# Kernel optimization log

Hardware: AMD Instinct MI355X
Metric: run time of the kernel (lower is better)

The kernel has to match this reference:

```python
import jax, jax.numpy as jnp
import numpy as np

N, M = 50000, 2048          # nodes, observations
E, O = 512, 256             # in_features_embed, in_features_obs
EPS = 1e-6


def setup_inputs() -> dict:
    key = jax.random.key(0)
    k1, k2, k3, k4, k5 = jax.random.split(key, 5)
    scale_e = 1.0 / np.sqrt(E)
    scale_o = 1.0 / np.sqrt(O)
    return {
        "node_feature": jax.random.normal(k1, (N, E), dtype=jnp.float32),
        "obs_feature": jax.random.normal(k2, (M, O), dtype=jnp.float32),
        # nn.Linear weights, stored as [out, in] like torch
        "W_q": jax.random.normal(k3, (E, E), dtype=jnp.float32) * scale_e,
        "W_k": jax.random.normal(k4, (E, O), dtype=jnp.float32) * scale_o,
        "W_v": jax.random.normal(k5, (E, O), dtype=jnp.float32) * scale_o,
        "ln_gamma": jnp.ones((E,), dtype=jnp.float32),
        "ln_beta": jnp.zeros((E,), dtype=jnp.float32),
    }


def layer_norm(x, gamma, beta, eps=EPS):
    mu = jnp.mean(x, axis=-1, keepdims=True)
    var = jnp.mean(jnp.square(x - mu), axis=-1, keepdims=True)
    return (x - mu) * jax.lax.rsqrt(var + eps) * gamma + beta


def reference(node_feature, obs_feature, W_q, W_k, W_v, ln_gamma, ln_beta):
    # projections (torch Linear: x @ W.T)
    q = node_feature @ W_q.T            # [N, E]
    k = obs_feature @ W_k.T             # [M, E]
    v = obs_feature @ W_v.T             # [M, E]
    # un-normalized cross-attention (no softmax), original association
    attn = q @ k.T                      # [N, M]
    out = attn @ v                      # [N, E]
    return layer_norm(out + node_feature, ln_gamma, ln_beta)
```

## Files before the change

kernel.cpp:

```cpp
#include <hip/hip_runtime.h>
#include <hip/hip_bf16.h>

#define NROWS 50000
#define MOBS  2048
#define EDIM  512
#define ODIM  256
#define BM2   128
#define NT2   391

typedef short s16x8 __attribute__((ext_vector_type(8)));
typedef float f32x4 __attribute__((ext_vector_type(4)));

typedef const __attribute__((address_space(1))) unsigned int* gptr_t;
typedef __attribute__((address_space(3))) unsigned int* lptr_t;

__device__ __forceinline__ unsigned short f32_to_bf16(float f) {
    unsigned int u = __float_as_uint(f);
    u += 0x7fffu + ((u >> 16) & 1u);
    return (unsigned short)(u >> 16);
}

__device__ __forceinline__ s16x8 pack8(f32x4 a, f32x4 b) {
    unsigned int p0, p1, p2, p3;
    asm("v_cvt_pk_bf16_f32 %0, %1, %2" : "=v"(p0) : "v"(a[0]), "v"(a[1]));
    asm("v_cvt_pk_bf16_f32 %0, %1, %2" : "=v"(p1) : "v"(a[2]), "v"(a[3]));
    asm("v_cvt_pk_bf16_f32 %0, %1, %2" : "=v"(p2) : "v"(b[0]), "v"(b[1]));
    asm("v_cvt_pk_bf16_f32 %0, %1, %2" : "=v"(p3) : "v"(b[2]), "v"(b[3]));
    union { unsigned int u[4]; s16x8 v; } r;
    r.u[0] = p0; r.u[1] = p1; r.u[2] = p2; r.u[3] = p3;
    return r.v;
}

__global__ __launch_bounds__(256) void chain1(const float* __restrict__ obs,
                                              const float* __restrict__ Wq,
                                              const float* __restrict__ Wk,
                                              float* __restrict__ Gp,
                                              float* __restrict__ Pp) {
    __shared__ float SA[16][68];
    __shared__ float SB[16][68];
    const int b = blockIdx.x;
    const float *A, *B;
    float* C;
    int lda, ldb, k_lo, k_hi, i0, j0;
    if (b < 128) {
        int z = b >> 4, tile = b & 15;
        i0 = (tile >> 2) * 64; j0 = (tile & 3) * 64;
        A = obs; B = obs; C = Gp + (size_t)z * 65536;
        lda = ODIM; ldb = ODIM;
        k_lo = z * 256; k_hi = k_lo + 256;
    } else {
        int i2 = b - 128;
        int z = i2 >> 5, tile = i2 & 31;
        i0 = (tile >> 2) * 64; j0 = (tile & 3) * 64;
        A = Wq; B = Wk; C = Pp + (size_t)z * 131072;
        lda = EDIM; ldb = ODIM;
        k_lo = z * 128; k_hi = k_lo + 128;
    }
    const int t  = threadIdx.x;
    const int tx = t & 15, ty = t >> 4;

    float acc[4][4];
#pragma unroll
    for (int a = 0; a < 4; ++a)
#pragma unroll
        for (int c2 = 0; c2 < 4; ++c2) acc[a][c2] = 0.f;

    for (int k0 = k_lo; k0 < k_hi; k0 += 16) {
#pragma unroll
        for (int r = 0; r < 4; ++r) {
            int idx = t + 256 * r;
            int mm = idx & 63, kk2 = idx >> 6;
            SA[kk2][mm] = A[(size_t)(k0 + kk2) * lda + i0 + mm];
        }
#pragma unroll
        for (int r = 0; r < 4; ++r) {
            int idx = t + 256 * r;
            int jj = idx & 63, kk2 = idx >> 6;
            SB[kk2][jj] = B[(size_t)(k0 + kk2) * ldb + j0 + jj];
        }
        __syncthreads();
#pragma unroll
        for (int kk2 = 0; kk2 < 16; ++kk2) {
            float4 a4 = *(const float4*)&SA[kk2][ty * 4];
            float4 b4 = *(const float4*)&SB[kk2][tx * 4];
            float av[4] = {a4.x, a4.y, a4.z, a4.w};
            float bv[4] = {b4.x, b4.y, b4.z, b4.w};
#pragma unroll
            for (int a = 0; a < 4; ++a)
#pragma unroll
                for (int c2 = 0; c2 < 4; ++c2) acc[a][c2] += av[a] * bv[c2];
        }
        __syncthreads();
    }
#pragma unroll
    for (int a = 0; a < 4; ++a) {
        float4 o = make_float4(acc[a][0], acc[a][1], acc[a][2], acc[a][3]);
        *(float4*)&C[(size_t)(i0 + ty * 4 + a) * ODIM + j0 + tx * 4] = o;
    }
}

__global__ __launch_bounds__(256) void chain2(const float* __restrict__ Gp,
                                              const float* __restrict__ Wv,
                                              float* __restrict__ GW) {
    __shared__ float SA[16][68];
    __shared__ float SB[16][68];
    const int t  = threadIdx.x;
    const int tx = t & 15, ty = t >> 4;
    const int i0 = blockIdx.y * 64, j0 = blockIdx.x * 64;

    float acc[4][4];
#pragma unroll
    for (int a = 0; a < 4; ++a)
#pragma unroll
        for (int c2 = 0; c2 < 4; ++c2) acc[a][c2] = 0.f;

    for (int k0 = 0; k0 < ODIM; k0 += 16) {
#pragma unroll
        for (int r = 0; r < 4; ++r) {
            int idx = t + 256 * r;
            int kk2 = idx & 15, mm = idx >> 4;
            size_t off = (size_t)(i0 + mm) * ODIM + k0 + kk2;
            float v = 0.f;
#pragma unroll
            for (int z = 0; z < 8; ++z) v += Gp[off + (size_t)z * 65536];
            SA[kk2][mm] = v;
        }
#pragma unroll
        for (int r = 0; r < 4; ++r) {
            int idx = t + 256 * r;
            int kk2 = idx & 15, jj = idx >> 4;
            SB[kk2][jj] = Wv[(size_t)(j0 + jj) * ODIM + k0 + kk2];
        }
        __syncthreads();
#pragma unroll
        for (int kk2 = 0; kk2 < 16; ++kk2) {
            float4 a4 = *(const float4*)&SA[kk2][ty * 4];
            float4 b4 = *(const float4*)&SB[kk2][tx * 4];
            float av[4] = {a4.x, a4.y, a4.z, a4.w};
            float bv[4] = {b4.x, b4.y, b4.z, b4.w};
#pragma unroll
            for (int a = 0; a < 4; ++a)
#pragma unroll
                for (int c2 = 0; c2 < 4; ++c2) acc[a][c2] += av[a] * bv[c2];
        }
        __syncthreads();
    }
#pragma unroll
    for (int a = 0; a < 4; ++a) {
        float4 o = make_float4(acc[a][0], acc[a][1], acc[a][2], acc[a][3]);
        *(float4*)&GW[(size_t)(i0 + ty * 4 + a) * EDIM + j0 + tx * 4] = o;
    }
}

__global__ __launch_bounds__(256) void chain3(const float* __restrict__ Pp,
                                              const float* __restrict__ GW,
                                              unsigned short* __restrict__ Uf) {
    __shared__ float SA[16][68];
    __shared__ float SB[16][68];
    const int t  = threadIdx.x;
    const int tx = t & 15, ty = t >> 4;
    const int i0 = blockIdx.y * 64, j0 = blockIdx.x * 64;

    float acc[4][4];
#pragma unroll
    for (int a = 0; a < 4; ++a)
#pragma unroll
        for (int c2 = 0; c2 < 4; ++c2) acc[a][c2] = 0.f;

    for (int k0 = 0; k0 < ODIM; k0 += 16) {
#pragma unroll
        for (int r = 0; r < 4; ++r) {
            int idx = t + 256 * r;
            int kk2 = idx & 15, mm = idx >> 4;
            size_t off = (size_t)(i0 + mm) * ODIM + k0 + kk2;
            float v = 0.f;
#pragma unroll
            for (int z = 0; z < 4; ++z) v += Pp[off + (size_t)z * 131072];
            SA[kk2][mm] = v;
        }
#pragma unroll
        for (int r = 0; r < 4; ++r) {
            int idx = t + 256 * r;
            int jj = idx & 63, kk2 = idx >> 6;
            SB[kk2][jj] = GW[(size_t)(k0 + kk2) * EDIM + j0 + jj];
        }
        __syncthreads();
#pragma unroll
        for (int kk2 = 0; kk2 < 16; ++kk2) {
            float4 a4 = *(const float4*)&SA[kk2][ty * 4];
            float4 b4 = *(const float4*)&SB[kk2][tx * 4];
            float av[4] = {a4.x, a4.y, a4.z, a4.w};
            float bv[4] = {b4.x, b4.y, b4.z, b4.w};
#pragma unroll
            for (int a = 0; a < 4; ++a)
#pragma unroll
                for (int c2 = 0; c2 < 4; ++c2) acc[a][c2] += av[a] * bv[c2];
        }
        __syncthreads();
    }
#pragma unroll
    for (int a = 0; a < 4; ++a)
#pragma unroll
        for (int c2 = 0; c2 < 4; ++c2) {
            int i = i0 + ty * 4 + a;
            int j = j0 + tx * 4 + c2;
            float v = acc[a][c2] + (i == j ? 1.f : 0.f);
            size_t idx = ((size_t)(((i >> 5) * 32 + (j >> 4)) * 64
                           + ((i >> 3) & 3) * 16 + (j & 15))) * 8 + (i & 7);
            Uf[idx] = f32_to_bf16(v);
        }
}

__global__ __launch_bounds__(512, 2) void gemm_pipe_ln(
    const float* __restrict__ node, const unsigned short* __restrict__ Uf,
    const float* __restrict__ gamma, const float* __restrict__ beta,
    float* __restrict__ out) {
    __shared__ char smem[147456];
    char* Areg = smem;
    char* Breg = smem + 49152;
    float* lds_s  = (float*)smem;
    float* lds_q  = (float*)smem + 512;
    float* lds_mu = (float*)smem + 1024;
    float* lds_rs = (float*)smem + 1152;

    const int t  = threadIdx.x;
    const int w  = t >> 6, l = t & 63;
    const int rg = w >> 2, cg = w & 3;
    const int lr = l & 15, lk = l >> 4;
    const int m0 = blockIdx.x * BM2;

    const int sr = w * 8 + (l >> 3);
    const int schunk = (l & 7) ^ ((l >> 3) & 7);
    int gr0 = m0 + sr;      if (gr0 > NROWS - 1) gr0 = NROWS - 1;
    int gr1 = m0 + sr + 64; if (gr1 > NROWS - 1) gr1 = NROWS - 1;
    const char* asrc0 = (const char*)node + (size_t)gr0 * 2048 + schunk * 16;
    const char* asrc1 = (const char*)node + (size_t)gr1 * 2048 + schunk * 16;
    const char* bsrc  = (const char*)Uf + (size_t)w * 4096 + (size_t)l * 16;

    auto dma = [&](int buf, int kt) {
        char* ad = Areg + buf * 16384 + w * 1024;
        __builtin_amdgcn_global_load_lds((gptr_t)(asrc0 + kt * 128),
                                         (lptr_t)ad, 16, 0, 0);
        __builtin_amdgcn_global_load_lds((gptr_t)(asrc1 + kt * 128),
                                         (lptr_t)(ad + 8192), 16, 0, 0);
        char* bd = Breg + buf * 32768 + w * 4096;
        const char* bs = bsrc + (size_t)kt * 32768;
#pragma unroll
        for (int j = 0; j < 4; ++j)
            __builtin_amdgcn_global_load_lds((gptr_t)(bs + j * 1024),
                                             (lptr_t)(bd + j * 1024), 16, 0, 0);
    };

    f32x4 acc[4][8];
#pragma unroll
    for (int mi = 0; mi < 4; ++mi)
#pragma unroll
        for (int ni = 0; ni < 8; ++ni)
            acc[mi][ni] = (f32x4){0.f, 0.f, 0.f, 0.f};

    auto compute = [&](int cur) {
        const char* bbase = Breg + cur * 32768 + cg * 8192 + l * 16;
        s16x8 bfr[8];
#pragma unroll
        for (int ni = 0; ni < 8; ++ni)
            bfr[ni] = *(const s16x8*)(bbase + ni * 1024);
        s16x8 afr[4];
#pragma unroll
        for (int mi = 0; mi < 4; ++mi) {
            int row = rg * 64 + mi * 16 + lr;
            const char* rb = Areg + cur * 16384 + row * 128;
            f32x4 a0 = *(const f32x4*)(rb + ((2 * lk)     ^ (lr & 7)) * 16);
            f32x4 a1 = *(const f32x4*)(rb + ((2 * lk + 1) ^ (lr & 7)) * 16);
            afr[mi] = pack8(a0, a1);
        }
#pragma unroll
        for (int mi = 0; mi < 4; ++mi)
#pragma unroll
            for (int ni = 0; ni < 8; ++ni)
                acc[mi][ni] = __builtin_amdgcn_mfma_f32_16x16x32_bf16(
                    afr[mi], bfr[ni], acc[mi][ni], 0, 0, 0);
    };

    dma(0, 0);
    dma(1, 1);

#pragma unroll 1
    for (int kt = 0; kt < 14; ++kt) {
        dma((kt + 2) % 3, kt + 2);
        asm volatile("s_waitcnt vmcnt(12)" ::: "memory");
        __builtin_amdgcn_sched_barrier(0);
        __builtin_amdgcn_s_barrier();
        compute(kt % 3);
        __builtin_amdgcn_s_barrier();
    }
    asm volatile("s_waitcnt vmcnt(6)" ::: "memory");
    __builtin_amdgcn_sched_barrier(0);
    __builtin_amdgcn_s_barrier();
    compute(14 % 3);
    __builtin_amdgcn_s_barrier();
    asm volatile("s_waitcnt vmcnt(0)" ::: "memory");
    __builtin_amdgcn_sched_barrier(0);
    __builtin_amdgcn_s_barrier();
    compute(15 % 3);
    __syncthreads();

#pragma unroll
    for (int mi = 0; mi < 4; ++mi) {
#pragma unroll
        for (int j = 0; j < 4; ++j) {
            float sm = 0.f, q = 0.f;
#pragma unroll
            for (int ni = 0; ni < 8; ++ni) {
                float v = acc[mi][ni][j];
                sm += v; q += v * v;
            }
#pragma unroll
            for (int off = 1; off < 16; off <<= 1) {
                sm += __shfl_xor(sm, off);
                q  += __shfl_xor(q, off);
            }
            if (lr == 0) {
                int row = rg * 64 + mi * 16 + lk * 4 + j;
                lds_s[cg * 128 + row] = sm;
                lds_q[cg * 128 + row] = q;
            }
        }
    }
    __syncthreads();
    if (t < 128) {
        float sm = lds_s[t] + lds_s[128 + t] + lds_s[256 + t] + lds_s[384 + t];
        float q  = lds_q[t] + lds_q[128 + t] + lds_q[256 + t] + lds_q[384 + t];
        float mu  = sm * (1.f / (float)EDIM);
        float var = q * (1.f / (float)EDIM) - mu * mu;
        lds_mu[t] = mu;
        lds_rs[t] = rsqrtf(var + 1e-6f);
    }
    __syncthreads();

    float gv[8], bv[8];
#pragma unroll
    for (int ni = 0; ni < 8; ++ni) {
        int col = cg * 128 + ni * 16 + lr;
        gv[ni] = gamma[col];
        bv[ni] = beta[col];
    }

#pragma unroll
    for (int mi = 0; mi < 4; ++mi) {
#pragma unroll
        for (int j = 0; j < 4; ++j) {
            int row = rg * 64 + mi * 16 + lk * 4 + j;
            int gr = m0 + row;
            if (gr < NROWS) {
                float mu = lds_mu[row], rs = lds_rs[row];
                float* op = out + (size_t)gr * EDIM + cg * 128 + lr;
#pragma unroll
                for (int ni = 0; ni < 8; ++ni)
                    op[ni * 16] = (acc[mi][ni][j] - mu) * rs * gv[ni] + bv[ni];
            }
        }
    }
}

extern "C" void kernel_launch(void* const* d_in, const int* in_sizes, int n_in,
                              void* d_out, int out_size, void* d_ws, size_t ws_size,
                              hipStream_t stream) {
    const float* node  = (const float*)d_in[0];
    const float* obs   = (const float*)d_in[1];
    const float* Wq    = (const float*)d_in[2];
    const float* Wk    = (const float*)d_in[3];
    const float* Wv    = (const float*)d_in[4];
    const float* gamma = (const float*)d_in[5];
    const float* beta  = (const float*)d_in[6];
    float* out = (float*)d_out;

    float* ws = (float*)d_ws;
    float* Gp = ws;
    float* Pp = Gp + 8 * 65536;
    float* GW = Pp + 4 * 131072;
    unsigned short* Uf = (unsigned short*)(GW + ODIM * EDIM);

    chain1<<<dim3(256), 256, 0, stream>>>(obs, Wq, Wk, Gp, Pp);
    chain2<<<dim3(8, 4), 256, 0, stream>>>(Gp, Wv, GW);
    chain3<<<dim3(8, 8), 256, 0, stream>>>(Pp, GW, Uf);
    gemm_pipe_ln<<<dim3(NT2), 512, 0, stream>>>(node, Uf, gamma, beta, out);
}
```

Baseline: 120.0 us.

## Unify small chain GEMMs with register-prefetched float4 loads and K=32 tiles

The three small fp32 GEMM kernels that build the fused weight matrix are replaced by one templated 64x64 tile routine. It loads tiles with float4 global reads, prefetches the next K-chunk into registers while the current chunk is computed, and doubles the K step to 32 so there are half as many barriers. The aim is to cut the latency-bound setup kernels that run before the main bf16 GEMM+LayerNorm kernel. In exchange it uses twice the shared memory and more registers, and the transposed shared-memory stores may cause bank conflicts.

Measured after the change: 115.4 us, median of 2. -3.8%, faster.

```diff
diff --git a/kernel.cpp b/kernel.cpp
--- a/kernel.cpp
+++ b/kernel.cpp
@@ -31,184 +31,175 @@
     return r.v;
 }
 
+template <int AKM, int BKM, int ZA, int NC, int FRAG>
+__device__ __forceinline__ void gemm64(const float* __restrict__ A, int lda, size_t zsA,
+                                       const float* __restrict__ B, int ldb,
+                                       void* __restrict__ Cv, int ldc,
+                                       int i0, int j0, int kbase,
+                                       float (*SA)[68], float (*SB)[68]) {
+    const int t  = threadIdx.x;
+    const int tx = t & 15, ty = t >> 4;
+
+    float4 ra[2][2], rb[2][2];
+
+    auto loadA = [&](float4 (&dst)[2], int c) {
+#pragma unroll
+        for (int r = 0; r < 2; ++r) {
+            int fi = t + r * 256;
+            if (AKM) {
+                int k = fi >> 4, m4 = (fi & 15) * 4;
+                dst[r] = *(const float4*)&A[(size_t)(kbase + c * 32 + k) * lda + i0 + m4];
+            } else {
+                int i = fi >> 3, kq = (fi & 7) * 4;
+                const float* p = &A[(size_t)(i0 + i) * lda + kbase + c * 32 + kq];
+                float4 v = *(const float4*)p;
+#pragma unroll
+                for (int z = 1; z < ZA; ++z) {
+                    float4 w2 = *(const float4*)(p + z * zsA);
+                    v.x += w2.x; v.y += w2.y; v.z += w2.z; v.w += w2.w;
+                }
+                dst[r] = v;
+            }
+        }
+    };
+    auto loadB = [&](float4 (&dst)[2], int c) {
+#pragma unroll
+        for (int r = 0; r < 2; ++r) {
+            int fi = t + r * 256;
+            if (BKM) {
+                int k = fi >> 4, j4 = (fi & 15) * 4;
+                dst[r] = *(const float4*)&B[(size_t)(kbase + c * 32 + k) * ldb + j0 + j4];
+            } else {
+                int j = fi >> 3, kq = (fi & 7) * 4;
+                dst[r] = *(const float4*)&B[(size_t)(j0 + j) * ldb + kbase + c * 32 + kq];
+            }
+        }
+    };
+    auto storeA = [&](float4 (&src)[2]) {
+#pragma unroll
+        for (int r = 0; r < 2; ++r) {
+            int fi = t + r * 256;
+            if (AKM) {
+                int k = fi >> 4, m4 = (fi & 15) * 4;
+                *(float4*)&SA[k][m4] = src[r];
+            } else {
+                int i = fi >> 3, kq = (fi & 7) * 4;
+                float4 v = src[r];
+                SA[kq][i] = v.x; SA[kq + 1][i] = v.y;
+                SA[kq + 2][i] = v.z; SA[kq + 3][i] = v.w;
+            }
+        }
+    };
+    auto storeB = [&](float4 (&src)[2]) {
+#pragma unroll
+        for (int r = 0; r < 2; ++r) {
+            int fi = t + r * 256;
+            if (BKM) {
+                int k = fi >> 4, j4 = (fi & 15) * 4;
+                *(float4*)&SB[k][j4] = src[r];
+            } else {
+                int j = fi >> 3, kq = (fi & 7) * 4;
+                float4 v = src[r];
+                SB[kq][j] = v.x; SB[kq + 1][j] = v.y;
+                SB[kq + 2][j] = v.z; SB[kq + 3][j] = v.w;
+            }
+        }
+    };
+
+    float acc[4][4];
+#pragma unroll
+    for (int a = 0; a < 4; ++a)
+#pragma unroll
+        for (int b2 = 0; b2 < 4; ++b2) acc[a][b2] = 0.f;
+
+    loadA(ra[0], 0);
+    loadB(rb[0], 0);
+
+#pragma unroll
+    for (int c = 0; c < NC; ++c) {
+        const int cur = c & 1, nxt = cur ^ 1;
+        if (c + 1 < NC) {
+            loadA(ra[nxt], c + 1);
+            loadB(rb[nxt], c + 1);
+        }
+        storeA(ra[cur]);
+        storeB(rb[cur]);
+        __syncthreads();
+#pragma unroll
+        for (int kk = 0; kk < 32; ++kk) {
+            float4 a4 = *(const float4*)&SA[kk][ty * 4];
+            float4 b4 = *(const float4*)&SB[kk][tx * 4];
+            float av[4] = {a4.x, a4.y, a4.z, a4.w};
+            float bv[4] = {b4.x, b4.y, b4.z, b4.w};
+#pragma unroll
+            for (int a = 0; a < 4; ++a)
+#pragma unroll
+                for (int b2 = 0; b2 < 4; ++b2) acc[a][b2] += av[a] * bv[b2];
+        }
+        __syncthreads();
+    }
+
+    if (FRAG) {
+        unsigned short* C = (unsigned short*)Cv;
+#pragma unroll
+        for (int a = 0; a < 4; ++a)
+#pragma unroll
+            for (int b2 = 0; b2 < 4; ++b2) {
+                int i = i0 + ty * 4 + a;
+                int j = j0 + tx * 4 + b2;
+                float v = acc[a][b2] + (i == j ? 1.f : 0.f);
+                size_t idx = ((size_t)(((i >> 5) * 32 + (j >> 4)) * 64
+                               + ((i >> 3) & 3) * 16 + (j & 15))) * 8 + (i & 7);
+                C[idx] = f32_to_bf16(v);
+            }
+    } else {
+        float* C = (float*)Cv;
+#pragma unroll
+        for (int a = 0; a < 4; ++a) {
+            float4 o = make_float4(acc[a][0], acc[a][1], acc[a][2], acc[a][3]);
+            *(float4*)&C[(size_t)(i0 + ty * 4 + a) * ldc + j0 + tx * 4] = o;
+        }
+    }
+}
+
 __global__ __launch_bounds__(256) void chain1(const float* __restrict__ obs,
                                               const float* __restrict__ Wq,
                                               const float* __restrict__ Wk,
                                               float* __restrict__ Gp,
                                               float* __restrict__ Pp) {
-    __shared__ float SA[16][68];
-    __shared__ float SB[16][68];
+    __shared__ float SA[32][68];
+    __shared__ float SB[32][68];
     const int b = blockIdx.x;
-    const float *A, *B;
-    float* C;
-    int lda, ldb, k_lo, k_hi, i0, j0;
     if (b < 128) {
         int z = b >> 4, tile = b & 15;
-        i0 = (tile >> 2) * 64; j0 = (tile & 3) * 64;
-        A = obs; B = obs; C = Gp + (size_t)z * 65536;
-        lda = ODIM; ldb = ODIM;
-        k_lo = z * 256; k_hi = k_lo + 256;
+        gemm64<1, 1, 1, 8, 0>(obs, ODIM, 0, obs, ODIM,
+                              Gp + (size_t)z * 65536, ODIM,
+                              (tile >> 2) * 64, (tile & 3) * 64, z * 256, SA, SB);
     } else {
         int i2 = b - 128;
         int z = i2 >> 5, tile = i2 & 31;
-        i0 = (tile >> 2) * 64; j0 = (tile & 3) * 64;
-        A = Wq; B = Wk; C = Pp + (size_t)z * 131072;
-        lda = EDIM; ldb = ODIM;
-        k_lo = z * 128; k_hi = k_lo + 128;
-    }
-    const int t  = threadIdx.x;
-    const int tx = t & 15, ty = t >> 4;
-
-    float acc[4][4];
-#pragma unroll
-    for (int a = 0; a < 4; ++a)
-#pragma unroll
-        for (int c2 = 0; c2 < 4; ++c2) acc[a][c2] = 0.f;
-
-    for (int k0 = k_lo; k0 < k_hi; k0 += 16) {
-#pragma unroll
-        for (int r = 0; r < 4; ++r) {
-            int idx = t + 256 * r;
-            int mm = idx & 63, kk2 = idx >> 6;
-            SA[kk2][mm] = A[(size_t)(k0 + kk2) * lda + i0 + mm];
-        }
-#pragma unroll
-        for (int r = 0; r < 4; ++r) {
-            int idx = t + 256 * r;
-            int jj = idx & 63, kk2 = idx >> 6;
-            SB[kk2][jj] = B[(size_t)(k0 + kk2) * ldb + j0 + jj];
-        }
-        __syncthreads();
-#pragma unroll
-        for (int kk2 = 0; kk2 < 16; ++kk2) {
-            float4 a4 = *(const float4*)&SA[kk2][ty * 4];
-            float4 b4 = *(const float4*)&SB[kk2][tx * 4];
-            float av[4] = {a4.x, a4.y, a4.z, a4.w};
-            float bv[4] = {b4.x, b4.y, b4.z, b4.w};
-#pragma unroll
-            for (int a = 0; a < 4; ++a)
-#pragma unroll
-                for (int c2 = 0; c2 < 4; ++c2) acc[a][c2] += av[a] * bv[c2];
-        }
-        __syncthreads();
-    }
-#pragma unroll
-    for (int a = 0; a < 4; ++a) {
-        float4 o = make_float4(acc[a][0], acc[a][1], acc[a][2], acc[a][3]);
-        *(float4*)&C[(size_t)(i0 + ty * 4 + a) * ODIM + j0 + tx * 4] = o;
+        gemm64<1, 1, 1, 4, 0>(Wq, EDIM, 0, Wk, ODIM,
+                              Pp + (size_t)z * 131072, ODIM,
+                              (tile >> 2) * 64, (tile & 3) * 64, z * 128, SA, SB);
     }
 }
 
 __global__ __launch_bounds__(256) void chain2(const float* __restrict__ Gp,
                                               const float* __restrict__ Wv,
                                               float* __restrict__ GW) {
-    __shared__ float SA[16][68];
-    __shared__ float SB[16][68];
-    const int t  = threadIdx.x;
-    const int tx = t & 15, ty = t >> 4;
-    const int i0 = blockIdx.y * 64, j0 = blockIdx.x * 64;
-
-    float acc[4][4];
-#pragma unroll
-    for (int a = 0; a < 4; ++a)
-#pragma unroll
-        for (int c2 = 0; c2 < 4; ++c2) acc[a][c2] = 0.f;
-
-    for (int k0 = 0; k0 < ODIM; k0 += 16) {
-#pragma unroll
-        for (int r = 0; r < 4; ++r) {
-            int idx = t + 256 * r;
-            int kk2 = idx & 15, mm = idx >> 4;
-            size_t off = (size_t)(i0 + mm) * ODIM + k0 + kk2;
-            float v = 0.f;
-#pragma unroll
-            for (int z = 0; z < 8; ++z) v += Gp[off + (size_t)z * 65536];
-            SA[kk2][mm] = v;
-        }
-#pragma unroll
-        for (int r = 0; r < 4; ++r) {
-            int idx = t + 256 * r;
-            int kk2 = idx & 15, jj = idx >> 4;
-            SB[kk2][jj] = Wv[(size_t)(j0 + jj) * ODIM + k0 + kk2];
-        }
-        __syncthreads();
-#pragma unroll
-        for (int kk2 = 0; kk2 < 16; ++kk2) {
-            float4 a4 = *(const float4*)&SA[kk2][ty * 4];
-            float4 b4 = *(const float4*)&SB[kk2][tx * 4];
-            float av[4] = {a4.x, a4.y, a4.z, a4.w};
-            float bv[4] = {b4.x, b4.y, b4.z, b4.w};
-#pragma unroll
-            for (int a = 0; a < 4; ++a)
-#pragma unroll
-                for (int c2 = 0; c2 < 4; ++c2) acc[a][c2] += av[a] * bv[c2];
-        }
-        __syncthreads();
-    }
-#pragma unroll
-    for (int a = 0; a < 4; ++a) {
-        float4 o = make_float4(acc[a][0], acc[a][1], acc[a][2], acc[a][3]);
-        *(float4*)&GW[(size_t)(i0 + ty * 4 + a) * EDIM + j0 + tx * 4] = o;
-    }
+    __shared__ float SA[32][68];
+    __shared__ float SB[32][68];
+    gemm64<0, 0, 8, 8, 0>(Gp, ODIM, 65536, Wv, ODIM, GW, EDIM,
+                          blockIdx.y * 64, blockIdx.x * 64, 0, SA, SB);
 }
 
 __global__ __launch_bounds__(256) void chain3(const float* __restrict__ Pp,
                                               const float* __restrict__ GW,
                                               unsigned short* __restrict__ Uf) {
-    __shared__ float SA[16][68];
-    __shared__ float SB[16][68];
-    const int t  = threadIdx.x;
-    const int tx = t & 15, ty = t >> 4;
-    const int i0 = blockIdx.y * 64, j0 = blockIdx.x * 64;
-
-    float acc[4][4];
-#pragma unroll
-    for (int a = 0; a < 4; ++a)
-#pragma unroll
-        for (int c2 = 0; c2 < 4; ++c2) acc[a][c2] = 0.f;
-
-    for (int k0 = 0; k0 < ODIM; k0 += 16) {
-#pragma unroll
-        for (int r = 0; r < 4; ++r) {
-            int idx = t + 256 * r;
-            int kk2 = idx & 15, mm = idx >> 4;
-            size_t off = (size_t)(i0 + mm) * ODIM + k0 + kk2;
-            float v = 0.f;
-#pragma unroll
-            for (int z = 0; z < 4; ++z) v += Pp[off + (size_t)z * 131072];
-            SA[kk2][mm] = v;
-        }
-#pragma unroll
-        for (int r = 0; r < 4; ++r) {
-            int idx = t + 256 * r;
-            int jj = idx & 63, kk2 = idx >> 6;
-            SB[kk2][jj] = GW[(size_t)(k0 + kk2) * EDIM + j0 + jj];
-        }
-        __syncthreads();
-#pragma unroll
-        for (int kk2 = 0; kk2 < 16; ++kk2) {
-            float4 a4 = *(const float4*)&SA[kk2][ty * 4];
-            float4 b4 = *(const float4*)&SB[kk2][tx * 4];
-            float av[4] = {a4.x, a4.y, a4.z, a4.w};
-            float bv[4] = {b4.x, b4.y, b4.z, b4.w};
-#pragma unroll
-            for (int a = 0; a < 4; ++a)
-#pragma unroll
-                for (int c2 = 0; c2 < 4; ++c2) acc[a][c2] += av[a] * bv[c2];
-        }
-        __syncthreads();
-    }
-#pragma unroll
-    for (int a = 0; a < 4; ++a)
-#pragma unroll
-        for (int c2 = 0; c2 < 4; ++c2) {
-            int i = i0 + ty * 4 + a;
-            int j = j0 + tx * 4 + c2;
-            float v = acc[a][c2] + (i == j ? 1.f : 0.f);
-            size_t idx = ((size_t)(((i >> 5) * 32 + (j >> 4)) * 64
-                           + ((i >> 3) & 3) * 16 + (j & 15))) * 8 + (i & 7);
-            Uf[idx] = f32_to_bf16(v);
-        }
+    __shared__ float SA[32][68];
+    __shared__ float SB[32][68];
+    gemm64<0, 1, 4, 8, 1>(Pp, ODIM, 131072, GW, EDIM, (void*)Uf, EDIM,
+                          blockIdx.y * 64, blockIdx.x * 64, 0, SA, SB);
 }
 
 __global__ __launch_bounds__(512, 2) void gemm_pipe_ln(
```
